# Kernel tuning notes

Measured on AMD Instinct MI355X. Metric: run time of the kernel, lower is better.

Reference implementation:

```python
import jax, jax.numpy as jnp
import numpy as np

N_NODES = 50000
N_EDGES = 800000
DIM = 128
HEADS = 4
NEG_SLOPE = 0.2
LN_EPS = 1e-5


def setup_inputs() -> dict:
    key = jax.random.key(0)
    ks = jax.random.split(key, 8)
    x = jax.random.normal(ks[0], (N_NODES, DIM), dtype=jnp.float32)
    edge_index = jax.random.randint(ks[1], (2, N_EDGES), 0, N_NODES, dtype=jnp.int32)
    W = jax.random.normal(ks[2], (DIM, DIM), dtype=jnp.float32) * (1.0 / np.sqrt(DIM))
    b = jnp.zeros((DIM,), dtype=jnp.float32)
    C = DIM // HEADS
    att_src = jax.random.normal(ks[3], (HEADS, C), dtype=jnp.float32) * 0.1
    att_dst = jax.random.normal(ks[4], (HEADS, C), dtype=jnp.float32) * 0.1
    ln_gamma = jnp.ones((DIM,), dtype=jnp.float32)
    ln_beta = jnp.zeros((DIM,), dtype=jnp.float32)
    prelu_w = jnp.full((1,), 0.25, dtype=jnp.float32)
    return {"x": x, "edge_index": edge_index, "W": W, "b": b,
            "att_src": att_src, "att_dst": att_dst,
            "ln_gamma": ln_gamma, "ln_beta": ln_beta, "prelu_w": prelu_w}


def reference(x, edge_index, W, b, att_src, att_dst, ln_gamma, ln_beta, prelu_w):
    N, D = x.shape
    H = HEADS
    C = D // H
    # shared linear transform (PyG GATConv lin_src == lin_dst for homogeneous input)
    xw = (x @ W).reshape(N, H, C)                      # [N,H,C]
    a_src = jnp.einsum('nhc,hc->nh', xw, att_src)      # [N,H]
    a_dst = jnp.einsum('nhc,hc->nh', xw, att_dst)      # [N,H]
    # add self loops (PyG default add_self_loops=True)
    loop = jnp.arange(N, dtype=edge_index.dtype)
    src = jnp.concatenate([edge_index[0], loop])       # [E+N]
    dst = jnp.concatenate([edge_index[1], loop])       # [E+N]
    # per-edge attention logits + segment softmax over destination
    alpha = jax.nn.leaky_relu(a_src[src] + a_dst[dst], NEG_SLOPE)   # [E+N,H]
    amax = jax.ops.segment_max(alpha, dst, num_segments=N)          # [N,H]
    alpha = jnp.exp(alpha - amax[dst])
    denom = jax.ops.segment_sum(alpha, dst, num_segments=N)         # [N,H]
    alpha = alpha / denom[dst]
    # weighted aggregation of source features
    msg = xw[src] * alpha[:, :, None]                               # [E+N,H,C]
    out = jax.ops.segment_sum(msg, dst, num_segments=N).reshape(N, D) + b
    # residual + LayerNorm + PReLU
    h = x + out
    mu = jnp.mean(h, axis=-1, keepdims=True)
    var = jnp.mean(jnp.square(h - mu), axis=-1, keepdims=True)
    h = (h - mu) * jax.lax.rsqrt(var + LN_EPS) * ln_gamma + ln_beta
    return jnp.where(h > 0, h, prelu_w[0] * h)
```

## Files before the change

### kernel.cpp

```cpp
#include <hip/hip_runtime.h>

#define NNODES 50000
#define NEDGES 800000
#define NEDGE4 200000
#define DIMF 128
#define NHEADS 4
#define NEG_SLOPE 0.2f
#define LN_EPS 1e-5f
#define SLOTS 64
#define NPERX 6250
#define NLB 782
#define SCB 2048

typedef int   v4i   __attribute__((ext_vector_type(4)));
typedef unsigned int v4u __attribute__((ext_vector_type(4)));
typedef float v2f   __attribute__((ext_vector_type(2)));
typedef float v4f   __attribute__((ext_vector_type(4)));
typedef unsigned int v2u __attribute__((ext_vector_type(2)));
typedef short bf16x8 __attribute__((ext_vector_type(8)));
typedef float f32x4  __attribute__((ext_vector_type(4)));
typedef unsigned short u16x8 __attribute__((ext_vector_type(8)));

__device__ __forceinline__ unsigned short f2bf(float f) {
    unsigned int u = __float_as_uint(f);
    u = (u + 0x7fffu + ((u >> 16) & 1u)) >> 16;
    return (unsigned short)u;
}
__device__ __forceinline__ float bf2f(unsigned short u) {
    return __uint_as_float(((unsigned int)u) << 16);
}

__global__ __launch_bounds__(256) void k_prep(
    const float* __restrict__ W, const int* __restrict__ esrc,
    const int* __restrict__ edst, unsigned short* __restrict__ WtG,
    int* __restrict__ cursor, unsigned int* __restrict__ epack)
{
    const int idx = blockIdx.x * 256 + threadIdx.x;
    if (idx < DIMF * DIMF) {
        const int k = idx >> 7, col = idx & 127;
        WtG[col * 136 + k] = f2bf(W[idx]);
    }
    if (idx < NNODES) cursor[idx] = 0;
    if (idx < NEDGES)
        epack[idx] = ((unsigned int)edst[idx] << 16) | (unsigned int)esrc[idx];
}

__global__ __launch_bounds__(256) void k_main(
    const float* __restrict__ x, const unsigned short* __restrict__ WtG,
    const float* __restrict__ att_src, const float* __restrict__ att_dst,
    unsigned char* __restrict__ xwb,
    float* __restrict__ asrc, float* __restrict__ adst,
    const unsigned int* __restrict__ epack,
    int* __restrict__ cursor, unsigned short* __restrict__ perm)
{
    __shared__ unsigned short WtL[64 * 136];
    __shared__ float sAttS[128], sAttD[128];
    const int tid = threadIdx.x;

    if (blockIdx.x < SCB) {
        const unsigned int lo = (blockIdx.x & 7) * NPERX, hi = lo + NPERX;
        const v4u* ep4 = (const v4u*)epack;
        const int stride = (SCB >> 3) * 256;
        for (int e = (blockIdx.x >> 3) * 256 + tid; e < NEDGE4; e += stride) {
            v4u p4 = __builtin_nontemporal_load(ep4 + e);
            #pragma unroll
            for (int c = 0; c < 4; ++c) {
                const unsigned int dd = p4[c] >> 16;
                if (dd >= lo && dd < hi) {
                    int p = atomicAdd(&cursor[dd], 1);
                    if (p < SLOTS)
                        perm[(size_t)dd * SLOTS + p] = (unsigned short)(p4[c] & 0xffffu);
                }
            }
        }
        return;
    }

    const int base = (blockIdx.x - SCB) * 64;

    if (tid < 128) sAttS[tid] = att_src[tid];
    else           sAttD[tid - 128] = att_dst[tid - 128];

    const int wv_   = tid >> 6;
    const int lane  = tid & 63;
    const int row16 = lane & 15;
    const int kg    = lane >> 4;
    const int grow_a = base + wv_ * 16 + row16;
    const int arow   = (grow_a < NNODES) ? grow_a : 0;

    bf16x8 af[4];
    #pragma unroll
    for (int ks = 0; ks < 4; ++ks) {
        const v4f* xr = (const v4f*)(x + (size_t)arow * DIMF + ks * 32 + kg * 8);
        const v4f xa = __builtin_nontemporal_load(xr);
        const v4f xb = __builtin_nontemporal_load(xr + 1);
        af[ks][0] = (short)f2bf(xa.x); af[ks][1] = (short)f2bf(xa.y);
        af[ks][2] = (short)f2bf(xa.z); af[ks][3] = (short)f2bf(xa.w);
        af[ks][4] = (short)f2bf(xb.x); af[ks][5] = (short)f2bf(xb.y);
        af[ks][6] = (short)f2bf(xb.z); af[ks][7] = (short)f2bf(xb.w);
    }

    f32x4 acc[8];
    #pragma unroll
    for (int ct = 0; ct < 8; ++ct) acc[ct] = (f32x4){0.f, 0.f, 0.f, 0.f};

    const v4u* g = (const v4u*)WtG;
    for (int hf = 0; hf < 2; ++hf) {
        __syncthreads();
        for (int i = tid; i < 1088; i += 256) {
            const v4u w = __builtin_nontemporal_load(g + hf * 1088 + i);
            ((v4u*)WtL)[i] = w;
        }
        __syncthreads();
        #pragma unroll
        for (int ks = 0; ks < 4; ++ks) {
            #pragma unroll
            for (int ct = 0; ct < 4; ++ct) {
                const bf16x8 bfr = *(const bf16x8*)&WtL[(ct * 16 + row16) * 136 + ks * 32 + kg * 8];
                acc[hf * 4 + ct] = __builtin_amdgcn_mfma_f32_16x16x32_bf16(af[ks], bfr, acc[hf * 4 + ct], 0, 0, 0);
            }
        }
    }

    __syncthreads();
    unsigned short* OutL = WtL;
    #pragma unroll
    for (int ct = 0; ct < 8; ++ct) {
        #pragma unroll
        for (int r = 0; r < 4; ++r)
            OutL[(wv_ * 16 + kg * 4 + r) * 136 + ct * 16 + row16] = f2bf(acc[ct][r]);
    }
    __syncthreads();

    const int rowD = tid >> 2, seg = tid & 3;
    const int growD = base + rowD;
    if (growD < NNODES) {
        float ps = 0.f, pd = 0.f;
        #pragma unroll
        for (int q = 0; q < 4; ++q) {
            const u16x8 v = *(const u16x8*)&OutL[rowD * 136 + seg * 32 + q * 8];
            #pragma unroll
            for (int j = 0; j < 8; ++j) {
                const float f = bf2f(v[j]);
                const int c = seg * 32 + q * 8 + j;
                ps += f * sAttS[c];
                pd += f * sAttD[c];
            }
        }
        __builtin_nontemporal_store(ps, &asrc[growD * NHEADS + seg]);
        __builtin_nontemporal_store(pd, &adst[growD * NHEADS + seg]);
    }

    #pragma unroll
    for (int it = 0; it < 4; ++it) {
        const int f = tid + it * 256;
        const int row = f >> 4;
        const int c8  = (f & 15) * 8;
        if (base + row < NNODES) {
            const u16x8 v = *(const u16x8*)&OutL[row * 136 + c8];
            unsigned int lo, hi;
            lo = __builtin_amdgcn_cvt_pk_fp8_f32(bf2f(v[0]), bf2f(v[1]), 0, false);
            lo = __builtin_amdgcn_cvt_pk_fp8_f32(bf2f(v[2]), bf2f(v[3]), lo, true);
            hi = __builtin_amdgcn_cvt_pk_fp8_f32(bf2f(v[4]), bf2f(v[5]), 0, false);
            hi = __builtin_amdgcn_cvt_pk_fp8_f32(bf2f(v[6]), bf2f(v[7]), hi, true);
            v2u pk; pk.x = lo; pk.y = hi;
            __builtin_nontemporal_store(pk, (v2u*)(xwb + (size_t)(base + row) * DIMF + c8));
        }
    }
}

__global__ __launch_bounds__(256) void k_gat(
    const float* __restrict__ x, const float* __restrict__ bias,
    const float4* __restrict__ asrc4, const float4* __restrict__ adst4,
    const unsigned short* __restrict__ xwb16,
    const int* __restrict__ cursor, const unsigned short* __restrict__ perm,
    const float* __restrict__ ln_g, const float* __restrict__ ln_b,
    const float* __restrict__ prelu_w, float* __restrict__ out)
{
    __shared__ unsigned short wlds[4][256];
    const int wid  = (blockIdx.x * 256 + threadIdx.x) >> 6;
    const int lane = threadIdx.x & 63;
    const int wv4  = threadIdx.x >> 6;
    if (wid >= NNODES) return;
    const int myh = lane >> 4;
    const int hb  = lane & 3;

    int cnt = cursor[wid];
    if (cnt > SLOTS) cnt = SLOTS;
    const int sidx = (lane < cnt) ? (int)perm[(size_t)wid * SLOTS + lane] : 0;

    const float4 dv = adst4[wid];
    {
        ushort4 wu = make_ushort4(0, 0, 0, 0);
        if (lane < cnt) {
            const float4 ae = asrc4[sidx];
            float l0 = ae.x + dv.x, l1 = ae.y + dv.y;
            float l2 = ae.z + dv.z, l3 = ae.w + dv.w;
            l0 = (l0 > 0.f) ? l0 : NEG_SLOPE * l0;
            l1 = (l1 > 0.f) ? l1 : NEG_SLOPE * l1;
            l2 = (l2 > 0.f) ? l2 : NEG_SLOPE * l2;
            l3 = (l3 > 0.f) ? l3 : NEG_SLOPE * l3;
            wu.x = f2bf(__expf(l0)); wu.y = f2bf(__expf(l1));
            wu.z = f2bf(__expf(l2)); wu.w = f2bf(__expf(l3));
        }
        *(ushort4*)&wlds[wv4][lane * 4] = wu;
    }

    const float ad_hb = (hb == 0) ? dv.x : (hb == 1) ? dv.y : (hb == 2) ? dv.z : dv.w;
    const float4 avw = asrc4[wid];
    const float as_hb = (hb == 0) ? avw.x : (hb == 1) ? avw.y : (hb == 2) ? avw.z : avw.w;
    float lgS = as_hb + ad_hb;
    lgS = (lgS > 0.f) ? lgS : NEG_SLOPE * lgS;
    const float wself_b = __expf(lgS);

    const float wself = __shfl(wself_b, myh);
    const v2f pself = __builtin_amdgcn_cvt_pk_f32_fp8(
        (unsigned int)xwb16[(size_t)wid * 64 + lane], false);
    float acc0 = wself * pself.x;
    float acc1 = wself * pself.y;
    float dsum = 0.f;

    const int jmax = (cnt + 15) >> 4;
    for (int j = 0; j < jmax; ++j) {
        const unsigned short wu = wlds[wv4][j * 64 + lane];
        const float wv = __uint_as_float(((unsigned)wu) << 16);
        dsum += wv;

        #pragma unroll
        for (int b = 0; b < 2; ++b) {
            const int ebase = j * 16 + b * 8;
            int s_[8]; float w_[8]; unsigned short v_[8];
            #pragma unroll
            for (int e = 0; e < 8; ++e) {
                s_[e] = __shfl(sidx, ebase + e);
                w_[e] = __shfl(wv, ((b * 8 + e) << 2) | myh);
            }
            #pragma unroll
            for (int e = 0; e < 8; ++e)
                v_[e] = xwb16[(size_t)s_[e] * 64 + lane];
            #pragma unroll
            for (int e = 0; e < 8; ++e) {
                const v2f p = __builtin_amdgcn_cvt_pk_f32_fp8((unsigned int)v_[e], false);
                acc0 += w_[e] * p.x;
                acc1 += w_[e] * p.y;
            }
        }
    }

    #pragma unroll
    for (int o = 4; o < 64; o <<= 1) dsum += __shfl_xor(dsum, o);
    const float wsum = __shfl(dsum + wself_b, myh);

    const float inv = 1.0f / wsum;
    const int c = lane * 2;
    const float2 xr = ((const float2*)x)[(size_t)wid * 64 + lane];
    float h0 = xr.x + acc0 * inv + bias[c];
    float h1 = xr.y + acc1 * inv + bias[c + 1];

    float s1 = h0 + h1, s2 = h0 * h0 + h1 * h1;
    #pragma unroll
    for (int o = 1; o < 64; o <<= 1) {
        s1 += __shfl_xor(s1, o);
        s2 += __shfl_xor(s2, o);
    }
    const float mu  = s1 * (1.f / 128.f);
    const float var = s2 * (1.f / 128.f) - mu * mu;
    const float r   = rsqrtf(var + LN_EPS);

    float g0 = (h0 - mu) * r * ln_g[c]     + ln_b[c];
    float g1 = (h1 - mu) * r * ln_g[c + 1] + ln_b[c + 1];
    const float pw = prelu_w[0];
    g0 = (g0 > 0.f) ? g0 : pw * g0;
    g1 = (g1 > 0.f) ? g1 : pw * g1;

    v2f gv; gv.x = g0; gv.y = g1;
    __builtin_nontemporal_store(gv, (v2f*)out + (size_t)wid * 64 + lane);
}

extern "C" void kernel_launch(void* const* d_in, const int* in_sizes, int n_in,
                              void* d_out, int out_size, void* d_ws, size_t ws_size,
                              hipStream_t stream)
{
    const float* x    = (const float*)d_in[0];
    const int*   eidx = (const int*)  d_in[1];
    const float* W    = (const float*)d_in[2];
    const float* bias = (const float*)d_in[3];
    const float* attS = (const float*)d_in[4];
    const float* attD = (const float*)d_in[5];
    const float* lng  = (const float*)d_in[6];
    const float* lnb  = (const float*)d_in[7];
    const float* pre  = (const float*)d_in[8];

    const int* esrc = eidx;
    const int* edst = eidx + NEDGES;

    char* wsp = (char*)d_ws;
    size_t off = 0;
    auto alloc = [&](size_t bytes) {
        char* p = wsp + off;
        off = (off + bytes + 255) & ~(size_t)255;
        return p;
    };
    unsigned char*  xwb    = (unsigned char*) alloc((size_t)NNODES * DIMF);
    float*          asrc   = (float*)         alloc((size_t)NNODES * NHEADS * 4);
    float*          adst   = (float*)         alloc((size_t)NNODES * NHEADS * 4);
    int*            cursor = (int*)           alloc((size_t)NNODES * 4);
    unsigned short* perm   = (unsigned short*)alloc((size_t)NNODES * SLOTS * 2);
    unsigned int*   epack  = (unsigned int*)  alloc((size_t)NEDGES * 4);
    unsigned short* WtG    = (unsigned short*)alloc((size_t)DIMF * 136 * 2);

    k_prep<<<dim3((NEDGES + 255) / 256), dim3(256), 0, stream>>>(
        W, esrc, edst, WtG, cursor, epack);

    k_main<<<dim3(SCB + NLB), dim3(256), 0, stream>>>(
        x, WtG, attS, attD, xwb, asrc, adst, epack, cursor, perm);

    k_gat<<<dim3((NNODES * 64 + 255) / 256), dim3(256), 0, stream>>>(
        x, bias, (const float4*)asrc, (const float4*)adst,
        (const unsigned short*)xwb, cursor, perm, lng, lnb, pre, (float*)d_out);
}
```

Before: 103.6 us.

## Drop edge packing pass, pad atomic cursors, reorder GEMM blocks first

Removes the epack precompute in k_prep: the scatter blocks now read esrc and edst directly, and k_prep shrinks to 196 blocks that only transpose W and zero the cursors. Cursor counters are padded to 16 ints (64 bytes) each, so atomics on neighbouring nodes no longer share a cache line. GEMM blocks are moved ahead of the scatter blocks in the grid, and several nontemporal loads and stores become ordinary ones. In exchange, each scatter block reads twice as many bytes of edge data, and the cursor array is 16 times larger.

```diff
diff --git a/kernel.cpp b/kernel.cpp
--- a/kernel.cpp
+++ b/kernel.cpp
@@ -11,6 +11,7 @@
 #define NPERX 6250
 #define NLB 782
 #define SCB 2048
+#define CPAD 16
 
 typedef int   v4i   __attribute__((ext_vector_type(4)));
 typedef unsigned int v4u __attribute__((ext_vector_type(4)));
@@ -30,19 +31,16 @@
     return __uint_as_float(((unsigned int)u) << 16);
 }
 
-__global__ __launch_bounds__(256) void k_prep(
-    const float* __restrict__ W, const int* __restrict__ esrc,
-    const int* __restrict__ edst, unsigned short* __restrict__ WtG,
-    int* __restrict__ cursor, unsigned int* __restrict__ epack)
+__global__ __launch_bounds__(256) void k_prep(const float* __restrict__ W,
+                                              unsigned short* __restrict__ WtG,
+                                              int* __restrict__ cursor)
 {
     const int idx = blockIdx.x * 256 + threadIdx.x;
     if (idx < DIMF * DIMF) {
         const int k = idx >> 7, col = idx & 127;
         WtG[col * 136 + k] = f2bf(W[idx]);
     }
-    if (idx < NNODES) cursor[idx] = 0;
-    if (idx < NEDGES)
-        epack[idx] = ((unsigned int)edst[idx] << 16) | (unsigned int)esrc[idx];
+    if (idx < NNODES) cursor[idx * CPAD] = 0;
 }
 
 __global__ __launch_bounds__(256) void k_main(
@@ -50,33 +48,35 @@
     const float* __restrict__ att_src, const float* __restrict__ att_dst,
     unsigned char* __restrict__ xwb,
     float* __restrict__ asrc, float* __restrict__ adst,
-    const unsigned int* __restrict__ epack,
+    const int* __restrict__ esrc, const int* __restrict__ edst,
     int* __restrict__ cursor, unsigned short* __restrict__ perm)
 {
     __shared__ unsigned short WtL[64 * 136];
     __shared__ float sAttS[128], sAttD[128];
     const int tid = threadIdx.x;
 
-    if (blockIdx.x < SCB) {
-        const unsigned int lo = (blockIdx.x & 7) * NPERX, hi = lo + NPERX;
-        const v4u* ep4 = (const v4u*)epack;
+    if (blockIdx.x >= NLB) {
+        const int vb = blockIdx.x - NLB;
+        const int lo = (vb & 7) * NPERX, hi = lo + NPERX;
+        const v4i* es4 = (const v4i*)esrc;
+        const v4i* ed4 = (const v4i*)edst;
         const int stride = (SCB >> 3) * 256;
-        for (int e = (blockIdx.x >> 3) * 256 + tid; e < NEDGE4; e += stride) {
-            v4u p4 = __builtin_nontemporal_load(ep4 + e);
+        for (int e = (vb >> 3) * 256 + tid; e < NEDGE4; e += stride) {
+            v4i d4 = __builtin_nontemporal_load(ed4 + e);
+            v4i s4 = __builtin_nontemporal_load(es4 + e);
             #pragma unroll
             for (int c = 0; c < 4; ++c) {
-                const unsigned int dd = p4[c] >> 16;
+                const int dd = d4[c], ss = s4[c];
                 if (dd >= lo && dd < hi) {
-                    int p = atomicAdd(&cursor[dd], 1);
-                    if (p < SLOTS)
-                        perm[(size_t)dd * SLOTS + p] = (unsigned short)(p4[c] & 0xffffu);
+                    int p = atomicAdd(&cursor[dd * CPAD], 1);
+                    if (p < SLOTS) perm[(size_t)dd * SLOTS + p] = (unsigned short)ss;
                 }
             }
         }
         return;
     }
 
-    const int base = (blockIdx.x - SCB) * 64;
+    const int base = blockIdx.x * 64;
 
     if (tid < 128) sAttS[tid] = att_src[tid];
     else           sAttD[tid - 128] = att_dst[tid - 128];
@@ -104,13 +104,11 @@
     #pragma unroll
     for (int ct = 0; ct < 8; ++ct) acc[ct] = (f32x4){0.f, 0.f, 0.f, 0.f};
 
-    const v4u* g = (const v4u*)WtG;
+    const uint4* g = (const uint4*)WtG;
     for (int hf = 0; hf < 2; ++hf) {
         __syncthreads();
-        for (int i = tid; i < 1088; i += 256) {
-            const v4u w = __builtin_nontemporal_load(g + hf * 1088 + i);
-            ((v4u*)WtL)[i] = w;
-        }
+        for (int i = tid; i < 1088; i += 256)
+            ((uint4*)WtL)[i] = g[hf * 1088 + i];
         __syncthreads();
         #pragma unroll
         for (int ks = 0; ks < 4; ++ks) {
@@ -147,8 +145,8 @@
                 pd += f * sAttD[c];
             }
         }
-        __builtin_nontemporal_store(ps, &asrc[growD * NHEADS + seg]);
-        __builtin_nontemporal_store(pd, &adst[growD * NHEADS + seg]);
+        asrc[growD * NHEADS + seg] = ps;
+        adst[growD * NHEADS + seg] = pd;
     }
 
     #pragma unroll
@@ -185,7 +183,7 @@
     const int myh = lane >> 4;
     const int hb  = lane & 3;
 
-    int cnt = cursor[wid];
+    int cnt = cursor[wid * CPAD];
     if (cnt > SLOTS) cnt = SLOTS;
     const int sidx = (lane < cnt) ? (int)perm[(size_t)wid * SLOTS + lane] : 0;
 
@@ -304,16 +302,14 @@
     unsigned char*  xwb    = (unsigned char*) alloc((size_t)NNODES * DIMF);
     float*          asrc   = (float*)         alloc((size_t)NNODES * NHEADS * 4);
     float*          adst   = (float*)         alloc((size_t)NNODES * NHEADS * 4);
-    int*            cursor = (int*)           alloc((size_t)NNODES * 4);
+    int*            cursor = (int*)           alloc((size_t)NNODES * CPAD * 4);
     unsigned short* perm   = (unsigned short*)alloc((size_t)NNODES * SLOTS * 2);
-    unsigned int*   epack  = (unsigned int*)  alloc((size_t)NEDGES * 4);
     unsigned short* WtG    = (unsigned short*)alloc((size_t)DIMF * 136 * 2);
 
-    k_prep<<<dim3((NEDGES + 255) / 256), dim3(256), 0, stream>>>(
-        W, esrc, edst, WtG, cursor, epack);
-
-    k_main<<<dim3(SCB + NLB), dim3(256), 0, stream>>>(
-        x, WtG, attS, attD, xwb, asrc, adst, epack, cursor, perm);
+    k_prep<<<dim3(196), dim3(256), 0, stream>>>(W, WtG, cursor);
+
+    k_main<<<dim3(NLB + SCB), dim3(256), 0, stream>>>(
+        x, WtG, attS, attD, xwb, asrc, adst, esrc, edst, cursor, perm);
 
     k_gat<<<dim3((NNODES * 64 + 255) / 256), dim3(256), 0, stream>>>(
         x, bias, (const float4*)asrc, (const float4*)adst,
```

New measurement: 101.0 us, median of 2. 2.5% less time.
